# Kernel optimization log

Measured on AMD Instinct MI355X. Metric: run time of the kernel, lower is better.

The kernel has to match this reference:

```python
import jax, jax.numpy as jnp
import numpy as np

L, C, F, K = 8192, 2048, 128, 257  # timesteps, input_size, filter_size, lag (odd => symmetric 'same' pad)
NY = 256  # number of overwritten channel rows


def setup_inputs() -> dict:
    key = jax.random.key(0)
    k1, k2, k3, k4 = jax.random.split(key, 4)
    x = jax.random.normal(k1, (L, C), dtype=jnp.float32)
    Yt = jax.random.randint(k2, (NY,), 0, C)
    # learned parameters (torch.rand -> uniform[0,1))
    g = jax.random.uniform(k3, (C, F), dtype=jnp.float32)
    kernel = jax.random.uniform(k4, (F, K), dtype=jnp.float32)
    return {"x": x, "Yt": Yt, "g": g, "kernel": kernel}


def reference(x, Yt, g, kernel):
    # synapse[c] is the per-channel 1D filter; the original builds a dense
    # (C, C, K) kernel whose only non-zero slices are the diagonal, so the
    # full conv1d is mathematically a depthwise (grouped) conv.
    synapse = jnp.matmul(g, kernel)          # (C, K)
    lhs = x.T[None]                          # (1, C, L)  NCH
    rhs = synapse[:, None, :]                # (C, 1, K)  OIH, groups=C
    pad = (kernel.shape[1] - 1) // 2         # torch padding='same', odd K
    out = jax.lax.conv_general_dilated(
        lhs, rhs,
        window_strides=(1,),
        padding=[(pad, pad)],
        feature_group_count=x.shape[1],
        dimension_numbers=("NCH", "OIH", "NCH"),
    )                                        # (1, C, L)
    # result[:, Yt, :] = x.T[Yt] : scatter-overwrite selected channel rows
    out = out.at[:, Yt, :].set(x.T[Yt][None])
    return out
```

## Files before the change

kernel.cpp:

```cpp
#include <hip/hip_runtime.h>

#define LL   8192
#define CC   2048
#define FF   128
#define KK   257
#define PAD  128

#define SROWP 328
#define NT   9
#define NCH  4
#define NW   4
#define ROWS 1352

typedef __bf16 bf16x8 __attribute__((ext_vector_type(8)));
typedef float  f32x4  __attribute__((ext_vector_type(4)));

static __device__ __forceinline__ unsigned short f2bf(float f) {
    unsigned u = __float_as_uint(f);
    u = (u + 0x7fffu + ((u >> 16) & 1u)) >> 16;
    return (unsigned short)u;
}

__global__ __launch_bounds__(256) void synb_kernel(const float* __restrict__ g,
                                                   const float* __restrict__ kern,
                                                   const int* __restrict__ Yt, int ny,
                                                   unsigned short* __restrict__ synEb) {
    __shared__ int sfl[4];
    const int c0 = blockIdx.x * 4;
    const int t  = threadIdx.x;
    if (t < 4) sfl[t] = 0;
    __syncthreads();
    for (int i = t; i < ny; i += 256) {
        int y = Yt[i];
        #pragma unroll
        for (int ii = 0; ii < 4; ++ii) if (y == c0 + ii) sfl[ii] = 1;
    }
    __syncthreads();
    const float* g0 = g + (size_t)(c0 + 0) * FF;
    const float* g1 = g + (size_t)(c0 + 1) * FF;
    const float* g2 = g + (size_t)(c0 + 2) * FF;
    const float* g3 = g + (size_t)(c0 + 3) * FF;
    const int fl0 = sfl[0], fl1 = sfl[1], fl2 = sfl[2], fl3 = sfl[3];
    for (int p = t; p < SROWP; p += 256) {
        const int kk = p - 32;
        float a0 = 0.f, a1 = 0.f, a2 = 0.f, a3 = 0.f;
        const bool inr = (kk >= 0) && (kk < KK);
        if (inr) {
            #pragma unroll 8
            for (int f = 0; f < FF; ++f) {
                float kv = kern[f * KK + kk];
                a0 += kv * g0[f];
                a1 += kv * g1[f];
                a2 += kv * g2[f];
                a3 += kv * g3[f];
            }
        }
        float dlt = (kk == PAD) ? 1.f : 0.f;
        float v0 = inr ? (fl0 ? dlt : a0) : 0.f;
        float v1 = inr ? (fl1 ? dlt : a1) : 0.f;
        float v2 = inr ? (fl2 ? dlt : a2) : 0.f;
        float v3 = inr ? (fl3 ? dlt : a3) : 0.f;
        synEb[(size_t)(c0 + 0) * SROWP + p] = f2bf(v0);
        synEb[(size_t)(c0 + 1) * SROWP + p] = f2bf(v1);
        synEb[(size_t)(c0 + 2) * SROWP + p] = f2bf(v2);
        synEb[(size_t)(c0 + 3) * SROWP + p] = f2bf(v3);
    }
}

static __device__ __forceinline__ void stage(const float* __restrict__ x,
                                             unsigned short (*buf)[ROWS],
                                             int W0, int c0, int t) {
    #pragma unroll
    for (int k = 0; k < 3; ++k) {
        int pp = (k << 8) + t;
        if (pp < 672) {
            int lg = W0 + (pp << 1) - 128;
            const float* sp = x + (size_t)lg * CC + c0;
            float4 a = make_float4(0.f, 0.f, 0.f, 0.f);
            float4 b = make_float4(0.f, 0.f, 0.f, 0.f);
            if ((unsigned)lg       < (unsigned)LL) a = *(const float4*)sp;
            if ((unsigned)(lg + 1) < (unsigned)LL) b = *(const float4*)(sp + CC);
            int gq = pp >> 2;
            int gp = gq ^ ((gq >> 3) & 7);
            int dw = (gp << 2) | (pp & 3);
            const float* pe = (const float*)&a;
            const float* po = (const float*)&b;
            #pragma unroll
            for (int c2 = 0; c2 < 4; ++c2) {
                unsigned val = (unsigned)f2bf(pe[c2]) | ((unsigned)f2bf(po[c2]) << 16);
                ((unsigned*)buf[c2])[dw] = val;
            }
        }
    }
}

__global__ __launch_bounds__(256, 4) void fused_conv(const float* __restrict__ x,
                                                     const unsigned short* __restrict__ synEb,
                                                     float* __restrict__ out) {
    __shared__ alignas(16) unsigned short xch[2][NCH][ROWS];
    __shared__ alignas(16) unsigned short synD[NCH][2][SROWP];
    const int t = threadIdx.x;

    const int d  = blockIdx.x;
    const int cg = ((d & 7) << 6) | (d >> 4);
    const int c0 = cg << 2;
    const int L0 = ((d >> 3) & 1) << 12;

    const int ci = t >> 6;
    const int ln = t & 63;
    const int n  = ln & 15, q4 = ln >> 4;
    const int gbase = (n << 1) + q4;
    const int ib  = (q4 << 3) - n + 32;
    const int par = ib & 1;
    const int e0  = (ib - par) >> 1;

    for (int u = t; u < NCH * 2 * SROWP; u += 256) {
        int ci2 = u / (2 * SROWP);
        int rem = u - ci2 * (2 * SROWP);
        int p   = (rem >= SROWP) ? 1 : 0;
        int idx = rem - (p ? SROWP : 0);
        int src = idx + p;
        if (src > SROWP - 1) src = SROWP - 1;
        synD[ci2][p][idx] = synEb[(size_t)(c0 + ci2) * SROWP + src];
    }
    stage(x, xch[0], L0, c0, t);
    __syncthreads();

    bf16x8 bfrag[NT];
    {
        const unsigned* bp = (const unsigned*)(synD[ci][par]) + e0;
        #pragma unroll
        for (int m = 0; m < NT; ++m) {
            union { unsigned dd[4]; bf16x8 v; } B;
            B.dd[0] = bp[(m << 4) + 0];
            B.dd[1] = bp[(m << 4) + 1];
            B.dd[2] = bp[(m << 4) + 2];
            B.dd[3] = bp[(m << 4) + 3];
            bfrag[m] = B.v;
        }
    }

    for (int w = 0; w < NW; ++w) {
        const int cur = w & 1;
        const int W0  = L0 + (w << 10);
        const char* xrow = (const char*)xch[cur][ci];

        f32x4 acc[4];
        #pragma unroll
        for (int s = 0; s < 4; ++s) acc[s] = (f32x4){0.f, 0.f, 0.f, 0.f};
        #pragma unroll
        for (int m = 0; m < NT; ++m) {
            #pragma unroll
            for (int s = 0; s < 4; ++s) {
                int g  = gbase + (s << 5) + (m << 2);
                int gp = g ^ ((g >> 3) & 7);
                union { int4 i4; bf16x8 v; } A;
                A.i4 = *(const int4*)(xrow + (gp << 4));
                acc[s] = __builtin_amdgcn_mfma_f32_16x16x32_bf16(A.v, bfrag[m], acc[s], 0, 0, 0);
            }
        }
        float* o = out + (size_t)(c0 + ci) * LL + W0 + (q4 << 6) + n;
        #pragma unroll
        for (int s = 0; s < 4; ++s) {
            #pragma unroll
            for (int r = 0; r < 4; ++r) o[(s << 8) + (r << 4)] = acc[s][r];
        }
        if (w + 1 < NW) stage(x, xch[cur ^ 1], W0 + 1024, c0, t);
        __syncthreads();
    }
}

extern "C" void kernel_launch(void* const* d_in, const int* in_sizes, int n_in,
                              void* d_out, int out_size, void* d_ws, size_t ws_size,
                              hipStream_t stream) {
    const float* x    = (const float*)d_in[0];
    const int*   Yt   = (const int*)  d_in[1];
    const float* g    = (const float*)d_in[2];
    const float* kern = (const float*)d_in[3];
    float* out = (float*)d_out;
    const int ny = in_sizes[1];

    unsigned short* synEb = (unsigned short*)d_ws;

    synb_kernel<<<CC / 4, 256, 0, stream>>>(g, kern, Yt, ny, synEb);
    fused_conv<<<1024, 256, 0, stream>>>(x, synEb, out);
}
```

Baseline: 153.0 us.

## Pre-transpose x to channel-major bf16 and stream conv directly from global

Adds a transpose kernel that converts x into a padded channel-major bf16 buffer in workspace. A new conv kernel then reads MFMA A-fragments straight from global memory without LDS staging, and builds B-fragments with funnel shifts instead of a parity-split LDS copy. The intent is to get rid of the strided per-timestep gathers and the LDS round trip in the fused kernel. The cost is an extra kernel launch and a full write-then-read of a roughly 35MB intermediate. The old fused kernel is kept as a fallback when the workspace is too small.

```diff
diff --git a/kernel.cpp b/kernel.cpp
--- a/kernel.cpp
+++ b/kernel.cpp
@@ -8,6 +8,10 @@
 
 #define SROWP 328
 #define NT   9
+
+#define LPAD   8512
+#define LTILES 133
+
 #define NCH  4
 #define NW   4
 #define ROWS 1352
@@ -67,9 +71,93 @@
     }
 }
 
-static __device__ __forceinline__ void stage(const float* __restrict__ x,
-                                             unsigned short (*buf)[ROWS],
-                                             int W0, int c0, int t) {
+__global__ __launch_bounds__(256) void xpose_kernel(const float* __restrict__ x,
+                                                    unsigned short* __restrict__ xT) {
+    __shared__ float tile[64][65];
+    const int t  = threadIdx.x;
+    const int lt = blockIdx.x;
+    const int C0 = blockIdx.y << 6;
+    const int lb = (lt << 6) - 128;
+    #pragma unroll
+    for (int it = 0; it < 16; ++it) {
+        int row = (it << 2) + (t >> 6);
+        int l = lb + row;
+        float v = 0.f;
+        if ((unsigned)l < (unsigned)LL) v = x[(size_t)l * CC + C0 + (t & 63)];
+        tile[row][t & 63] = v;
+    }
+    __syncthreads();
+    #pragma unroll
+    for (int h = 0; h < 2; ++h) {
+        int c_loc = (t >> 3) + (h << 5);
+        int l0    = (t & 7) << 3;
+        unsigned dd[4];
+        #pragma unroll
+        for (int i = 0; i < 4; ++i) {
+            unsigned lo = f2bf(tile[l0 + 2 * i][c_loc]);
+            unsigned hi = f2bf(tile[l0 + 2 * i + 1][c_loc]);
+            dd[i] = lo | (hi << 16);
+        }
+        *(uint4*)(xT + (size_t)(C0 + c_loc) * LPAD + (lt << 6) + l0) =
+            make_uint4(dd[0], dd[1], dd[2], dd[3]);
+    }
+}
+
+__global__ __launch_bounds__(256, 4) void conv_stream(const unsigned short* __restrict__ xT,
+                                                      const unsigned short* __restrict__ synEb,
+                                                      float* __restrict__ out) {
+    const int t  = threadIdx.x;
+    const int c  = (blockIdx.y << 2) + (t >> 6);
+    const int Lb = blockIdx.x << 11;
+    const int ln = t & 63;
+    const int n = ln & 15, q4 = ln >> 4;
+
+    const int ib  = (q4 << 3) - n + 32;
+    const int dwb = ib >> 1;
+    const int sh  = (ib & 1) << 4;
+    const unsigned* rp = (const unsigned*)(synEb + (size_t)c * SROWP) + dwb;
+    bf16x8 bfrag[NT];
+    #pragma unroll
+    for (int m = 0; m < NT; ++m) {
+        unsigned w0 = rp[(m << 4) + 0], w1 = rp[(m << 4) + 1], w2 = rp[(m << 4) + 2],
+                 w3 = rp[(m << 4) + 3], w4 = rp[(m << 4) + 4];
+        union { unsigned dd[4]; bf16x8 v; } B;
+        B.dd[0] = (unsigned)((((unsigned long long)w1 << 32) | w0) >> sh);
+        B.dd[1] = (unsigned)((((unsigned long long)w2 << 32) | w1) >> sh);
+        B.dd[2] = (unsigned)((((unsigned long long)w3 << 32) | w2) >> sh);
+        B.dd[3] = (unsigned)((((unsigned long long)w4 << 32) | w3) >> sh);
+        bfrag[m] = B.v;
+    }
+
+    const unsigned short* xrow = xT + (size_t)c * LPAD + Lb + (n << 4) + (q4 << 3);
+
+    #pragma unroll
+    for (int it = 0; it < 2; ++it) {
+        const unsigned short* xr = xrow + (it << 10);
+        f32x4 acc[4];
+        #pragma unroll
+        for (int s = 0; s < 4; ++s) acc[s] = (f32x4){0.f, 0.f, 0.f, 0.f};
+        #pragma unroll
+        for (int m = 0; m < NT; ++m) {
+            #pragma unroll
+            for (int s = 0; s < 4; ++s) {
+                union { int4 i4; bf16x8 v; } A;
+                A.i4 = *(const int4*)(xr + (s << 8) + (m << 5));
+                acc[s] = __builtin_amdgcn_mfma_f32_16x16x32_bf16(A.v, bfrag[m], acc[s], 0, 0, 0);
+            }
+        }
+        float* o = out + (size_t)c * LL + Lb + (it << 10) + (q4 << 6) + n;
+        #pragma unroll
+        for (int s = 0; s < 4; ++s) {
+            #pragma unroll
+            for (int r = 0; r < 4; ++r) o[(s << 8) + (r << 4)] = acc[s][r];
+        }
+    }
+}
+
+static __device__ __forceinline__ void stage_fb(const float* __restrict__ x,
+                                                unsigned short (*buf)[ROWS],
+                                                int W0, int c0, int t) {
     #pragma unroll
     for (int k = 0; k < 3; ++k) {
         int pp = (k << 8) + t;
@@ -94,18 +182,16 @@
     }
 }
 
-__global__ __launch_bounds__(256, 4) void fused_conv(const float* __restrict__ x,
-                                                     const unsigned short* __restrict__ synEb,
-                                                     float* __restrict__ out) {
+__global__ __launch_bounds__(256, 4) void fused_conv_fb(const float* __restrict__ x,
+                                                        const unsigned short* __restrict__ synEb,
+                                                        float* __restrict__ out) {
     __shared__ alignas(16) unsigned short xch[2][NCH][ROWS];
     __shared__ alignas(16) unsigned short synD[NCH][2][SROWP];
     const int t = threadIdx.x;
-
     const int d  = blockIdx.x;
     const int cg = ((d & 7) << 6) | (d >> 4);
     const int c0 = cg << 2;
     const int L0 = ((d >> 3) & 1) << 12;
-
     const int ci = t >> 6;
     const int ln = t & 63;
     const int n  = ln & 15, q4 = ln >> 4;
@@ -123,7 +209,7 @@
         if (src > SROWP - 1) src = SROWP - 1;
         synD[ci2][p][idx] = synEb[(size_t)(c0 + ci2) * SROWP + src];
     }
-    stage(x, xch[0], L0, c0, t);
+    stage_fb(x, xch[0], L0, c0, t);
     __syncthreads();
 
     bf16x8 bfrag[NT];
@@ -144,7 +230,6 @@
         const int cur = w & 1;
         const int W0  = L0 + (w << 10);
         const char* xrow = (const char*)xch[cur][ci];
-
         f32x4 acc[4];
         #pragma unroll
         for (int s = 0; s < 4; ++s) acc[s] = (f32x4){0.f, 0.f, 0.f, 0.f};
@@ -165,7 +250,7 @@
             #pragma unroll
             for (int r = 0; r < 4; ++r) o[(s << 8) + (r << 4)] = acc[s][r];
         }
-        if (w + 1 < NW) stage(x, xch[cur ^ 1], W0 + 1024, c0, t);
+        if (w + 1 < NW) stage_fb(x, xch[cur ^ 1], W0 + 1024, c0, t);
         __syncthreads();
     }
 }
@@ -180,8 +265,17 @@
     float* out = (float*)d_out;
     const int ny = in_sizes[1];
 
+    const size_t synBytes = (size_t)CC * SROWP * 2;
+    const size_t xTBytes  = (size_t)CC * LPAD * 2;
     unsigned short* synEb = (unsigned short*)d_ws;
+    unsigned short* xT    = (unsigned short*)((char*)d_ws + synBytes);
 
     synb_kernel<<<CC / 4, 256, 0, stream>>>(g, kern, Yt, ny, synEb);
-    fused_conv<<<1024, 256, 0, stream>>>(x, synEb, out);
-}
+
+    if (ws_size >= synBytes + xTBytes) {
+        xpose_kernel<<<dim3(LTILES, CC / 64), 256, 0, stream>>>(x, xT);
+        conv_stream<<<dim3(LL / 2048, CC / 4), 256, 0, stream>>>(xT, synEb, out);
+    } else {
+        fused_conv_fb<<<1024, 256, 0, stream>>>(x, synEb, out);
+    }
+}
```

New measurement: 167.7 us. 1.1x slower.
